# Optimization experiments

Hardware: AMD Instinct MI355X
Metric: run time of the kernel (lower is better)

## Reference

```python
import jax, jax.numpy as jnp
import numpy as np

COMMITMENT_COST = 0.25


def setup_inputs() -> dict:
    key = jax.random.key(0)
    k1, k2 = jax.random.split(key)
    x = jax.random.normal(k1, (32, 1024, 512), dtype=jnp.float32)
    codebook = jax.random.normal(k2, (8192, 512), dtype=jnp.float32)
    return {"x": x, "codebook": codebook}


def reference(x, codebook):
    D = codebook.shape[1]
    flat = x.reshape(-1, D)                                   # [N, D]
    # squared L2 distances: ||f||^2 + ||c||^2 - 2 f c^T
    distances = (
        jnp.sum(flat * flat, axis=1, keepdims=True)
        + jnp.sum(codebook * codebook, axis=1)
        - 2.0 * jnp.matmul(flat, codebook.T)                   # [N, K]
    )
    encoding_indices = jnp.argmin(distances, axis=1)           # [N]
    quantized = codebook[encoding_indices].reshape(x.shape)    # [.., D]
    commitment_loss = COMMITMENT_COST * jnp.mean(
        (jax.lax.stop_gradient(quantized) - x) ** 2
    )
    # straight-through estimator
    quantized_st = x + jax.lax.stop_gradient(quantized - x)
    return (quantized_st, commitment_loss)
```

## Files before the change

### kernel.cpp

```cpp
#include <hip/hip_runtime.h>
#include <stdint.h>

#define N_TOT 32768
#define DDIM  512
#define KCB   8192
#define NSPLIT 4
#define COLS_SPLIT (KCB / NSPLIT)
#define BN 128
#define BC 128
#define BKD 64
#define NTILES (COLS_SPLIT / BC)
#define MARGIN 0.15f

#define RB3 16
#define RP3 32
#define RSLOTS 64
#define RGRID3 2048

typedef _Float16 half8 __attribute__((ext_vector_type(8)));
typedef float    floatx4 __attribute__((ext_vector_type(4)));

typedef const __attribute__((address_space(1))) unsigned int* gas_ptr;
typedef __attribute__((address_space(3))) unsigned int* las_ptr;
__device__ __forceinline__ void gld_lds16(void* l, const void* g) {
    __builtin_amdgcn_global_load_lds((gas_ptr)g, (las_ptr)l, 16, 0, 0);
}

__device__ __forceinline__ unsigned long long shfl_xor_u64(unsigned long long v, int m) {
    unsigned int lo = (unsigned int)v, hi = (unsigned int)(v >> 32);
    lo = __shfl_xor(lo, m, 64);
    hi = __shfl_xor(hi, m, 64);
    return ((unsigned long long)hi << 32) | lo;
}

__global__ __launch_bounds__(256) void convert_x_kernel(
    const float* __restrict__ x, _Float16* __restrict__ xh) {
    size_t i = ((size_t)blockIdx.x * 256 + threadIdx.x) * 8;
    float4 v0 = *(const float4*)(x + i);
    float4 v1 = *(const float4*)(x + i + 4);
    half8 h;
    h[0] = (_Float16)v0.x; h[1] = (_Float16)v0.y; h[2] = (_Float16)v0.z; h[3] = (_Float16)v0.w;
    h[4] = (_Float16)v1.x; h[5] = (_Float16)v1.y; h[6] = (_Float16)v1.z; h[7] = (_Float16)v1.w;
    *(half8*)(xh + i) = h;
}

__global__ __launch_bounds__(256) void convert_cb_kernel(
    const float* __restrict__ cb, _Float16* __restrict__ cbh, float* __restrict__ cnorm) {
    int row = blockIdx.x * 4 + (threadIdx.x >> 6);
    int lane = threadIdx.x & 63;
    const float* src = cb + (size_t)row * DDIM + lane * 8;
    float4 v0 = *(const float4*)src;
    float4 v1 = *(const float4*)(src + 4);
    half8 h;
    h[0] = (_Float16)v0.x; h[1] = (_Float16)v0.y; h[2] = (_Float16)v0.z; h[3] = (_Float16)v0.w;
    h[4] = (_Float16)v1.x; h[5] = (_Float16)v1.y; h[6] = (_Float16)v1.z; h[7] = (_Float16)v1.w;
    *(half8*)(cbh + (size_t)row * DDIM + lane * 8) = h;
    float s = v0.x*v0.x + v0.y*v0.y + v0.z*v0.z + v0.w*v0.w
            + v1.x*v1.x + v1.y*v1.y + v1.z*v1.z + v1.w*v1.w;
#pragma unroll
    for (int off = 32; off > 0; off >>= 1) s += __shfl_down(s, off, 64);
    if (lane == 0) cnorm[row] = s;
}

__global__ __launch_bounds__(256, 2) void gemm_argmin_kernel(
    const _Float16* __restrict__ xh, const _Float16* __restrict__ cbh,
    const float* __restrict__ cnorm,
    float* __restrict__ sb1, int* __restrict__ si1, float* __restrict__ sb2) {

    __shared__ __align__(16) _Float16 smem[16384];
    _Float16* As = smem;
    _Float16* Bs = smem + 8192;

    const int tid = threadIdx.x;
    const int wave = tid >> 6;
    const int lane = tid & 63;
    const int rowHalf = wave >> 1;
    const int colHalf = wave & 1;
    const int l15 = lane & 15;
    const int quad = lane >> 4;

    const int row0 = blockIdx.x * BN;
    const int colBase = blockIdx.y * COLS_SPLIT;

    float b1[16], b2[16];
    int   i1[16];
#pragma unroll
    for (int s = 0; s < 16; ++s) { b1[s] = 3.402823466e38f; b2[s] = 3.402823466e38f; i1[s] = 0; }

    for (int tile = 0; tile < NTILES; ++tile) {
        const int col0 = colBase + tile * BC;
        floatx4 acc[4][4];
#pragma unroll
        for (int i = 0; i < 4; ++i)
#pragma unroll
            for (int j = 0; j < 4; ++j)
                acc[i][j] = (floatx4){0.f, 0.f, 0.f, 0.f};

        for (int d0 = 0; d0 < DDIM; d0 += BKD) {
            __syncthreads();
#pragma unroll
            for (int r = 0; r < 4; ++r) {
                int c = wave * 256 + r * 64 + lane;
                int ar = c >> 3;
                int q  = (c & 7) ^ (ar & 7);
                gld_lds16(As + (wave * 256 + r * 64) * 8,
                          xh + (((size_t)(row0 + ar)) << 9) + d0 + q * 8);
            }
#pragma unroll
            for (int r = 0; r < 4; ++r) {
                int c = wave * 256 + r * 64 + lane;
                int br = c >> 3;
                int q  = (c & 7) ^ (br & 7);
                gld_lds16(Bs + (wave * 256 + r * 64) * 8,
                          cbh + (((size_t)(col0 + br)) << 9) + d0 + q * 8);
            }
            __syncthreads();
#pragma unroll
            for (int kh = 0; kh < 2; ++kh) {
                half8 af[4], bf[4];
#pragma unroll
                for (int i = 0; i < 4; ++i) {
                    int rr = rowHalf * 64 + i * 16 + l15;
                    int qs = (kh * 4 + quad) ^ (rr & 7);
                    af[i] = *(const half8*)(As + rr * 64 + qs * 8);
                }
#pragma unroll
                for (int j = 0; j < 4; ++j) {
                    int cc = colHalf * 64 + j * 16 + l15;
                    int qs = (kh * 4 + quad) ^ (cc & 7);
                    bf[j] = *(const half8*)(Bs + cc * 64 + qs * 8);
                }
#pragma unroll
                for (int i = 0; i < 4; ++i)
#pragma unroll
                    for (int j = 0; j < 4; ++j)
                        acc[i][j] = __builtin_amdgcn_mfma_f32_16x16x32_f16(
                            af[i], bf[j], acc[i][j], 0, 0, 0);
            }
        }
#pragma unroll
        for (int j = 0; j < 4; ++j) {
            int col = col0 + colHalf * 64 + j * 16 + l15;
            float cn = cnorm[col];
#pragma unroll
            for (int i = 0; i < 4; ++i) {
#pragma unroll
                for (int r = 0; r < 4; ++r) {
                    float s = fmaf(-2.0f, acc[i][j][r], cn);
                    int slot = i * 4 + r;
                    if (s < b1[slot]) { b2[slot] = b1[slot]; b1[slot] = s; i1[slot] = col; }
                    else if (s < b2[slot]) b2[slot] = s;
                }
            }
        }
    }

#pragma unroll
    for (int m = 1; m < 16; m <<= 1) {
#pragma unroll
        for (int s = 0; s < 16; ++s) {
            float ob1 = __shfl_xor(b1[s], m, 64);
            float ob2 = __shfl_xor(b2[s], m, 64);
            int   oi1 = __shfl_xor(i1[s], m, 64);
            if (ob1 < b1[s] || (ob1 == b1[s] && oi1 < i1[s])) {
                b2[s] = fminf(b1[s], ob2);
                b1[s] = ob1; i1[s] = oi1;
            } else {
                b2[s] = fminf(b2[s], ob1);
            }
        }
    }

    __syncthreads();
    float* mb1 = (float*)smem;
    float* mb2 = mb1 + 256;
    int*   mi1 = (int*)(mb2 + 256);
    if (l15 == 0) {
#pragma unroll
        for (int s = 0; s < 16; ++s) {
            int row = rowHalf * 64 + (s >> 2) * 16 + quad * 4 + (s & 3);
            mb1[colHalf * 128 + row] = b1[s];
            mb2[colHalf * 128 + row] = b2[s];
            mi1[colHalf * 128 + row] = i1[s];
        }
    }
    __syncthreads();
    if (tid < 128) {
        float a1 = mb1[tid], a2 = mb2[tid]; int ai = mi1[tid];
        float c1 = mb1[128 + tid], c2 = mb2[128 + tid]; int ci = mi1[128 + tid];
        float r1, r2; int ri;
        if (c1 < a1 || (c1 == a1 && ci < ai)) { r1 = c1; ri = ci; r2 = fminf(a1, c2); }
        else { r1 = a1; ri = ai; r2 = fminf(a2, c1); }
        size_t o = (size_t)blockIdx.y * N_TOT + row0 + tid;
        sb1[o] = r1; si1[o] = ri; sb2[o] = r2;
    }
}

__global__ __launch_bounds__(256) void merge_kernel(
    const float* __restrict__ sb1, const int* __restrict__ si1, const float* __restrict__ sb2,
    int* __restrict__ indices, int* __restrict__ flags,
    int* __restrict__ list, int* __restrict__ count,
    unsigned long long* __restrict__ result) {
    int n = blockIdx.x * 256 + threadIdx.x;
    float b1 = sb1[n]; int i1 = si1[n]; float b2 = sb2[n];
#pragma unroll
    for (int s = 1; s < NSPLIT; ++s) {
        float ob1 = sb1[(size_t)s * N_TOT + n];
        int   oi1 = si1[(size_t)s * N_TOT + n];
        float ob2 = sb2[(size_t)s * N_TOT + n];
        if (ob1 < b1 || (ob1 == b1 && oi1 < i1)) { b2 = fminf(b1, ob2); b1 = ob1; i1 = oi1; }
        else b2 = fminf(b2, ob1);
    }
    indices[n] = i1;
    result[n] = 0xFFFFFFFFFFFFFFFFull;
    int f = (b2 - b1 < MARGIN) ? 1 : 0;
    flags[n] = f;
    if (f) { int pos = atomicAdd(count, 1); list[pos] = n; }
}

__global__ __launch_bounds__(256) void repair3_kernel(
    const float* __restrict__ x, const float* __restrict__ cb,
    const float* __restrict__ cnorm, const int* __restrict__ list,
    const int* __restrict__ count, unsigned long long* __restrict__ result) {
    __shared__ __align__(16) float xs[RB3][512];
    __shared__ unsigned long long red[RB3][4];
    const int tid = threadIdx.x;
    const int lane = tid & 63;
    const int wv = tid >> 6;
    const int part = blockIdx.x & (RP3 - 1);
    const int slot0 = blockIdx.x >> 5;
    const int cnt = *count;
    const int nbatch = (cnt + RB3 - 1) / RB3;
    const int k = part * 256 + tid;
    const float cn = cnorm[k];
    const float* crow = cb + (size_t)k * 512;

    for (int batch = slot0; batch < nbatch; batch += RSLOTS) {
        const int rb = min(RB3, cnt - batch * RB3);
        __syncthreads();
        for (int t = tid; t < rb * 128; t += 256) {
            int b = t >> 7, d4 = t & 127;
            int n = list[batch * RB3 + b];
            ((float4*)xs[b])[d4] = ((const float4*)(x + ((size_t)n << 9)))[d4];
        }
        __syncthreads();

        float d0[RB3], d1[RB3], d2[RB3], d3[RB3];
#pragma unroll
        for (int b = 0; b < RB3; ++b) { d0[b] = 0.f; d1[b] = 0.f; d2[b] = 0.f; d3[b] = 0.f; }

        for (int t = 0; t < 512; t += 16) {
            float4 c0 = *(const float4*)(crow + t);
            float4 c1 = *(const float4*)(crow + t + 4);
            float4 c2 = *(const float4*)(crow + t + 8);
            float4 c3 = *(const float4*)(crow + t + 12);
#pragma unroll
            for (int b = 0; b < RB3; ++b) {
                float4 x0 = *(const float4*)&xs[b][t];
                float4 x1 = *(const float4*)&xs[b][t + 4];
                float4 x2 = *(const float4*)&xs[b][t + 8];
                float4 x3 = *(const float4*)&xs[b][t + 12];
                d0[b] = fmaf(c0.x, x0.x, d0[b]);  d0[b] = fmaf(c0.y, x0.y, d0[b]);
                d0[b] = fmaf(c0.z, x0.z, d0[b]);  d0[b] = fmaf(c0.w, x0.w, d0[b]);
                d1[b] = fmaf(c1.x, x1.x, d1[b]);  d1[b] = fmaf(c1.y, x1.y, d1[b]);
                d1[b] = fmaf(c1.z, x1.z, d1[b]);  d1[b] = fmaf(c1.w, x1.w, d1[b]);
                d2[b] = fmaf(c2.x, x2.x, d2[b]);  d2[b] = fmaf(c2.y, x2.y, d2[b]);
                d2[b] = fmaf(c2.z, x2.z, d2[b]);  d2[b] = fmaf(c2.w, x2.w, d2[b]);
                d3[b] = fmaf(c3.x, x3.x, d3[b]);  d3[b] = fmaf(c3.y, x3.y, d3[b]);
                d3[b] = fmaf(c3.z, x3.z, d3[b]);  d3[b] = fmaf(c3.w, x3.w, d3[b]);
            }
        }

#pragma unroll
        for (int b = 0; b < RB3; ++b) {
            float s = cn - 2.f * ((d0[b] + d1[b]) + (d2[b] + d3[b]));
            unsigned int sb = __float_as_uint(s);
            sb = (sb & 0x80000000u) ? ~sb : (sb | 0x80000000u);
            unsigned long long p = ((unsigned long long)sb << 32) | (unsigned int)k;
#pragma unroll
            for (int m = 32; m > 0; m >>= 1) {
                unsigned long long o = shfl_xor_u64(p, m);
                if (o < p) p = o;
            }
            if (lane == 0) red[b][wv] = p;
        }
        __syncthreads();
        if (tid < RB3) {
            unsigned long long p = red[tid][0];
            if (red[tid][1] < p) p = red[tid][1];
            if (red[tid][2] < p) p = red[tid][2];
            if (red[tid][3] < p) p = red[tid][3];
            if (tid < rb) {
                int n = list[batch * RB3 + tid];
                atomicMin(&result[n], p);
            }
        }
    }
}

__global__ __launch_bounds__(256) void fixup_kernel(
    const int* __restrict__ flags, const unsigned long long* __restrict__ result,
    int* __restrict__ indices) {
    int n = blockIdx.x * 256 + threadIdx.x;
    if (flags[n]) indices[n] = (int)(result[n] & 0xFFFFFFFFu);
}

__global__ void cnorm_kernel(const float* __restrict__ cb, float* __restrict__ cnorm) {
    int wave = (blockIdx.x * blockDim.x + threadIdx.x) >> 6;
    int lane = threadIdx.x & 63;
    if (wave >= KCB) return;
    const float* row = cb + (size_t)wave * DDIM;
    float s = 0.f;
#pragma unroll
    for (int j = 0; j < DDIM / 64; ++j) { float v = row[lane + 64 * j]; s += v * v; }
#pragma unroll
    for (int off = 32; off > 0; off >>= 1) s += __shfl_down(s, off, 64);
    if (lane == 0) cnorm[wave] = s;
}

#define FBN 64
#define FBD 32
#define FLDA (FBN + 4)
__global__ __launch_bounds__(256) void argmin_fp32_kernel(
    const float* __restrict__ x, const float* __restrict__ cb,
    const float* __restrict__ cnorm, int* __restrict__ indices) {
    __shared__ float As[FBD][FLDA];
    __shared__ float Bs[FBD][FLDA];
    __shared__ float redv[FBN][16];
    __shared__ int   redi[FBN][16];
    const int tid = threadIdx.x;
    const int tx = tid & 15, ty = tid >> 4;
    const int row0 = blockIdx.x * FBN;
    float best[4]; int bidx[4];
#pragma unroll
    for (int i = 0; i < 4; ++i) { best[i] = 3.402823466e+38f; bidx[i] = KCB; }
    for (int k0 = 0; k0 < KCB; k0 += 64) {
        float acc[4][4] = {};
        for (int d0 = 0; d0 < DDIM; d0 += FBD) {
#pragma unroll
            for (int t = 0; t < 2; ++t) {
                int q = tid + t * 256, rr = q >> 3, dq = q & 7;
                float4 v = *(const float4*)(x + (size_t)(row0 + rr) * DDIM + d0 + dq * 4);
                As[dq*4+0][rr] = v.x; As[dq*4+1][rr] = v.y; As[dq*4+2][rr] = v.z; As[dq*4+3][rr] = v.w;
                float4 w = *(const float4*)(cb + (size_t)(k0 + rr) * DDIM + d0 + dq * 4);
                Bs[dq*4+0][rr] = w.x; Bs[dq*4+1][rr] = w.y; Bs[dq*4+2][rr] = w.z; Bs[dq*4+3][rr] = w.w;
            }
            __syncthreads();
#pragma unroll
            for (int d = 0; d < FBD; ++d) {
                float4 av = *(const float4*)&As[d][ty * 4];
                float4 bv = *(const float4*)&Bs[d][tx * 4];
                float a[4] = {av.x, av.y, av.z, av.w}, b[4] = {bv.x, bv.y, bv.z, bv.w};
#pragma unroll
                for (int i = 0; i < 4; ++i)
#pragma unroll
                    for (int j = 0; j < 4; ++j) acc[i][j] += a[i] * b[j];
            }
            __syncthreads();
        }
#pragma unroll
        for (int j = 0; j < 4; ++j) {
            int k = k0 + tx * 4 + j;
            float cn = cnorm[k];
#pragma unroll
            for (int i = 0; i < 4; ++i) {
                float s = cn - 2.0f * acc[i][j];
                if (s < best[i] || (s == best[i] && k < bidx[i])) { best[i] = s; bidx[i] = k; }
            }
        }
    }
#pragma unroll
    for (int i = 0; i < 4; ++i) { redv[ty*4+i][tx] = best[i]; redi[ty*4+i][tx] = bidx[i]; }
    __syncthreads();
    if (tid < FBN) {
        float bv = redv[tid][0]; int bi = redi[tid][0];
#pragma unroll
        for (int t = 1; t < 16; ++t) {
            float v = redv[tid][t]; int ii = redi[tid][t];
            if (v < bv || (v == bv && ii < bi)) { bv = v; bi = ii; }
        }
        indices[row0 + tid] = bi;
    }
}

__global__ __launch_bounds__(256) void output_kernel(
    const float* __restrict__ x, const float* __restrict__ cb,
    const int* __restrict__ indices, float* __restrict__ out,
    float* __restrict__ loss_acc) {
    size_t base = ((size_t)blockIdx.x * blockDim.x + threadIdx.x) * 16;
    int n = (int)(base >> 9);
    int d = (int)(base & 511);
    int idx = indices[n];
    const float* cr = cb + (size_t)idx * DDIM + d;
    const float* xr = x + base;
    float* orow = out + base;
    float lsum = 0.f;
#pragma unroll
    for (int t = 0; t < 4; ++t) {
        float4 q  = *(const float4*)(cr + t * 4);
        float4 xv = *(const float4*)(xr + t * 4);
        float dx0 = q.x - xv.x, dx1 = q.y - xv.y, dx2 = q.z - xv.z, dx3 = q.w - xv.w;
        float4 o;
        o.x = xv.x + dx0; o.y = xv.y + dx1; o.z = xv.z + dx2; o.w = xv.w + dx3;
        *(float4*)(orow + t * 4) = o;
        lsum += dx0*dx0 + dx1*dx1 + dx2*dx2 + dx3*dx3;
    }
#pragma unroll
    for (int off = 32; off > 0; off >>= 1) lsum += __shfl_down(lsum, off, 64);
    __shared__ float wsum[4];
    int lane = threadIdx.x & 63, wv = threadIdx.x >> 6;
    if (lane == 0) wsum[wv] = lsum;
    __syncthreads();
    if (threadIdx.x == 0) atomicAdd(loss_acc, wsum[0] + wsum[1] + wsum[2] + wsum[3]);
}

__global__ void finalize_kernel(const float* __restrict__ loss_acc, float* __restrict__ out_loss) {
    *out_loss = (*loss_acc) * (0.25f / (float)((size_t)N_TOT * DDIM));
}

extern "C" void kernel_launch(void* const* d_in, const int* in_sizes, int n_in,
                              void* d_out, int out_size, void* d_ws, size_t ws_size,
                              hipStream_t stream) {
    const float* x  = (const float*)d_in[0];
    const float* cb = (const float*)d_in[1];
    float* out = (float*)d_out;

    char* ws = (char*)d_ws;
    float* loss_acc = (float*)ws;
    int*   count    = (int*)(ws + 8);
    int*   indices  = (int*)(ws + 256);
    int*   flags    = (int*)(ws + 256 + 131072);
    float* cnorm    = (float*)(ws + 256 + 2 * 131072);
    int*   list     = (int*)(ws + 256 + 2 * 131072 + 32768);
    unsigned long long* result =
        (unsigned long long*)(ws + 256 + 3 * 131072 + 32768);
    size_t off = 256 + 3 * 131072 + 32768 + 262144;
    _Float16* xh  = (_Float16*)(ws + off);
    _Float16* cbh = (_Float16*)(ws + off + (size_t)N_TOT * DDIM * 2);
    size_t soff = off + (size_t)N_TOT * DDIM * 2 + (size_t)KCB * DDIM * 2;
    float* sb1 = (float*)(ws + soff);
    int*   si1 = (int*)(ws + soff + (size_t)NSPLIT * N_TOT * 4);
    float* sb2 = (float*)(ws + soff + (size_t)NSPLIT * N_TOT * 8);
    size_t need = soff + (size_t)NSPLIT * N_TOT * 12;

    hipMemsetAsync(ws, 0, 16, stream);
    if (ws_size >= need) {
        convert_x_kernel<<<(N_TOT * DDIM) / (256 * 8), 256, 0, stream>>>(x, xh);
        convert_cb_kernel<<<KCB / 4, 256, 0, stream>>>(cb, cbh, cnorm);
        dim3 grid(N_TOT / BN, NSPLIT);
        gemm_argmin_kernel<<<grid, 256, 0, stream>>>(xh, cbh, cnorm, sb1, si1, sb2);
        merge_kernel<<<N_TOT / 256, 256, 0, stream>>>(sb1, si1, sb2, indices, flags,
                                                      list, count, result);
        repair3_kernel<<<RGRID3, 256, 0, stream>>>(x, cb, cnorm, list, count, result);
        fixup_kernel<<<N_TOT / 256, 256, 0, stream>>>(flags, result, indices);
    } else {
        cnorm_kernel<<<KCB / 4, 256, 0, stream>>>(cb, cnorm);
        argmin_fp32_kernel<<<N_TOT / FBN, 256, 0, stream>>>(x, cb, cnorm, indices);
    }
    output_kernel<<<((size_t)N_TOT * DDIM) / (256 * 16), 256, 0, stream>>>(
        x, cb, indices, out, loss_acc);
    finalize_kernel<<<1, 1, 0, stream>>>(loss_acc, out + (size_t)N_TOT * DDIM);
}
```

Measured before the change: 878.7 us.

## Double-buffer LDS tiles in GEMM-argmin and swizzle workgroup order across XCDs

Turns the GEMM-argmin main loop into a flattened, double-buffered pipeline. The next K-slab is prefetched into a second LDS buffer while MFMAs run on the current one, so each step needs one barrier instead of two. The launch becomes a 1D grid with a block index remap, likely to group blocks per XCD for better L2 reuse of the codebook. It also changes the repair kernel's RB3 and RSLOTS constants. The cost is doubled LDS (64KB per block), which may limit occupancy below the requested 2 blocks per CU.

```diff
diff --git a/kernel.cpp b/kernel.cpp
--- a/kernel.cpp
+++ b/kernel.cpp
@@ -10,11 +10,12 @@
 #define BC 128
 #define BKD 64
 #define NTILES (COLS_SPLIT / BC)
+#define NSTEPS (NTILES * 8)
 #define MARGIN 0.15f
 
-#define RB3 16
+#define RB3 32
 #define RP3 32
-#define RSLOTS 64
+#define RSLOTS (RGRID3 / RP3)
 #define RGRID3 2048
 
 typedef _Float16 half8 __attribute__((ext_vector_type(8)));
@@ -67,9 +68,7 @@
     const float* __restrict__ cnorm,
     float* __restrict__ sb1, int* __restrict__ si1, float* __restrict__ sb2) {
 
-    __shared__ __align__(16) _Float16 smem[16384];
-    _Float16* As = smem;
-    _Float16* Bs = smem + 8192;
+    __shared__ __align__(16) _Float16 smem[32768];
 
     const int tid = threadIdx.x;
     const int wave = tid >> 6;
@@ -79,81 +78,99 @@
     const int l15 = lane & 15;
     const int quad = lane >> 4;
 
-    const int row0 = blockIdx.x * BN;
-    const int colBase = blockIdx.y * COLS_SPLIT;
+    const int orig = blockIdx.x;
+    const int wg = ((orig & 7) << 7) | (orig >> 3);
+    const int bx = wg & 255;
+    const int by = wg >> 8;
+    const int row0 = bx * BN;
+    const int colBase = by * COLS_SPLIT;
 
     float b1[16], b2[16];
     int   i1[16];
 #pragma unroll
     for (int s = 0; s < 16; ++s) { b1[s] = 3.402823466e38f; b2[s] = 3.402823466e38f; i1[s] = 0; }
 
-    for (int tile = 0; tile < NTILES; ++tile) {
-        const int col0 = colBase + tile * BC;
-        floatx4 acc[4][4];
-#pragma unroll
-        for (int i = 0; i < 4; ++i)
-#pragma unroll
-            for (int j = 0; j < 4; ++j)
-                acc[i][j] = (floatx4){0.f, 0.f, 0.f, 0.f};
-
-        for (int d0 = 0; d0 < DDIM; d0 += BKD) {
-            __syncthreads();
-#pragma unroll
-            for (int r = 0; r < 4; ++r) {
-                int c = wave * 256 + r * 64 + lane;
-                int ar = c >> 3;
-                int q  = (c & 7) ^ (ar & 7);
-                gld_lds16(As + (wave * 256 + r * 64) * 8,
-                          xh + (((size_t)(row0 + ar)) << 9) + d0 + q * 8);
-            }
-#pragma unroll
-            for (int r = 0; r < 4; ++r) {
-                int c = wave * 256 + r * 64 + lane;
-                int br = c >> 3;
-                int q  = (c & 7) ^ (br & 7);
-                gld_lds16(Bs + (wave * 256 + r * 64) * 8,
-                          cbh + (((size_t)(col0 + br)) << 9) + d0 + q * 8);
-            }
-            __syncthreads();
-#pragma unroll
-            for (int kh = 0; kh < 2; ++kh) {
-                half8 af[4], bf[4];
+#define STAGE(par, tilev, d0v) do {                                             \
+        _Float16* Asb = smem + (par) * 16384;                                   \
+        _Float16* Bsb = Asb + 8192;                                             \
+        const int col0s = colBase + (tilev) * BC;                               \
+        _Pragma("unroll")                                                       \
+        for (int r = 0; r < 4; ++r) {                                           \
+            int c = wave * 256 + r * 64 + lane;                                 \
+            int ar = c >> 3;                                                    \
+            int q  = (c & 7) ^ (ar & 7);        \
+            gld_lds16(Asb + (wave * 256 + r * 64) * 8,                          \
+                      xh + (((size_t)(row0 + ar)) << 9) + (d0v) + q * 8);       \
+            gld_lds16(Bsb + (wave * 256 + r * 64) * 8,                          \
+                      cbh + (((size_t)(col0s + ar)) << 9) + (d0v) + q * 8);     \
+        }                                                                       \
+    } while (0)
+
+    floatx4 acc[4][4];
+#pragma unroll
+    for (int i = 0; i < 4; ++i)
+#pragma unroll
+        for (int j = 0; j < 4; ++j)
+            acc[i][j] = (floatx4){0.f, 0.f, 0.f, 0.f};
+
+    STAGE(0, 0, 0);
+    __syncthreads();
+
+    for (int s = 0; s < NSTEPS; ++s) {
+        const int par = s & 1;
+        if (s + 1 < NSTEPS) {
+            STAGE((s + 1) & 1, (s + 1) >> 3, ((s + 1) & 7) * BKD);
+        }
+        _Float16* As = smem + par * 16384;
+        _Float16* Bs = As + 8192;
+#pragma unroll
+        for (int kh = 0; kh < 2; ++kh) {
+            half8 af[4], bf[4];
+#pragma unroll
+            for (int i = 0; i < 4; ++i) {
+                int rr = rowHalf * 64 + i * 16 + l15;
+                int qs = (kh * 4 + quad) ^ (rr & 7);
+                af[i] = *(const half8*)(As + rr * 64 + qs * 8);
+            }
+#pragma unroll
+            for (int j = 0; j < 4; ++j) {
+                int cc = colHalf * 64 + j * 16 + l15;
+                int qs = (kh * 4 + quad) ^ (cc & 7);
+                bf[j] = *(const half8*)(Bs + cc * 64 + qs * 8);
+            }
+#pragma unroll
+            for (int i = 0; i < 4; ++i)
+#pragma unroll
+                for (int j = 0; j < 4; ++j)
+                    acc[i][j] = __builtin_amdgcn_mfma_f32_16x16x32_f16(
+                        af[i], bf[j], acc[i][j], 0, 0, 0);
+        }
+        if ((s & 7) == 7) {
+            const int col0 = colBase + (s >> 3) * BC;
+#pragma unroll
+            for (int j = 0; j < 4; ++j) {
+                int col = col0 + colHalf * 64 + j * 16 + l15;
+                float cn = cnorm[col];
 #pragma unroll
                 for (int i = 0; i < 4; ++i) {
-                    int rr = rowHalf * 64 + i * 16 + l15;
-                    int qs = (kh * 4 + quad) ^ (rr & 7);
-                    af[i] = *(const half8*)(As + rr * 64 + qs * 8);
+#pragma unroll
+                    for (int r = 0; r < 4; ++r) {
+                        float sc = fmaf(-2.0f, acc[i][j][r], cn);
+                        int slot = i * 4 + r;
+                        if (sc < b1[slot]) { b2[slot] = b1[slot]; b1[slot] = sc; i1[slot] = col; }
+                        else if (sc < b2[slot]) b2[slot] = sc;
+                    }
                 }
-#pragma unroll
-                for (int j = 0; j < 4; ++j) {
-                    int cc = colHalf * 64 + j * 16 + l15;
-                    int qs = (kh * 4 + quad) ^ (cc & 7);
-                    bf[j] = *(const half8*)(Bs + cc * 64 + qs * 8);
-                }
-#pragma unroll
-                for (int i = 0; i < 4; ++i)
-#pragma unroll
-                    for (int j = 0; j < 4; ++j)
-                        acc[i][j] = __builtin_amdgcn_mfma_f32_16x16x32_f16(
-                            af[i], bf[j], acc[i][j], 0, 0, 0);
-            }
-        }
-#pragma unroll
-        for (int j = 0; j < 4; ++j) {
-            int col = col0 + colHalf * 64 + j * 16 + l15;
-            float cn = cnorm[col];
-#pragma unroll
-            for (int i = 0; i < 4; ++i) {
-#pragma unroll
-                for (int r = 0; r < 4; ++r) {
-                    float s = fmaf(-2.0f, acc[i][j][r], cn);
-                    int slot = i * 4 + r;
-                    if (s < b1[slot]) { b2[slot] = b1[slot]; b1[slot] = s; i1[slot] = col; }
-                    else if (s < b2[slot]) b2[slot] = s;
-                }
-            }
-        }
-    }
+            }
+#pragma unroll
+            for (int i = 0; i < 4; ++i)
+#pragma unroll
+                for (int j = 0; j < 4; ++j)
+                    acc[i][j] = (floatx4){0.f, 0.f, 0.f, 0.f};
+        }
+        __syncthreads();
+    }
+#undef STAGE
 
 #pragma unroll
     for (int m = 1; m < 16; m <<= 1) {
@@ -171,7 +188,6 @@
         }
     }
 
-    __syncthreads();
     float* mb1 = (float*)smem;
     float* mb2 = mb1 + 256;
     int*   mi1 = (int*)(mb2 + 256);
@@ -191,7 +207,7 @@
         float r1, r2; int ri;
         if (c1 < a1 || (c1 == a1 && ci < ai)) { r1 = c1; ri = ci; r2 = fminf(a1, c2); }
         else { r1 = a1; ri = ai; r2 = fminf(a2, c1); }
-        size_t o = (size_t)blockIdx.y * N_TOT + row0 + tid;
+        size_t o = (size_t)by * N_TOT + row0 + tid;
         sb1[o] = r1; si1[o] = ri; sb2[o] = r2;
     }
 }
@@ -447,8 +463,8 @@
     if (ws_size >= need) {
         convert_x_kernel<<<(N_TOT * DDIM) / (256 * 8), 256, 0, stream>>>(x, xh);
         convert_cb_kernel<<<KCB / 4, 256, 0, stream>>>(cb, cbh, cnorm);
-        dim3 grid(N_TOT / BN, NSPLIT);
-        gemm_argmin_kernel<<<grid, 256, 0, stream>>>(xh, cbh, cnorm, sb1, si1, sb2);
+        gemm_argmin_kernel<<<(N_TOT / BN) * NSPLIT, 256, 0, stream>>>(
+            xh, cbh, cnorm, sb1, si1, sb2);
         merge_kernel<<<N_TOT / 256, 256, 0, stream>>>(sb1, si1, sb2, indices, flags,
                                                       list, count, result);
         repair3_kernel<<<RGRID3, 256, 0, stream>>>(x, cb, cnorm, list, count, result);
```

Result: faster. 834.3 us (-5.1%).
